# Kernel optimization log

Measured on AMD Instinct MI355X. Metric: run time of the kernel, lower is better.

Reference implementation:

```python
import jax, jax.numpy as jnp
import numpy as np

D_MODEL = 1024
N_HEADS = 16
D_K = D_MODEL // N_HEADS
THETA = 10000.0
SEQ = 2048
BATCH = 2


def setup_inputs() -> dict:
    key = jax.random.key(0)
    ks = jax.random.split(key, 5)
    std = (2.0 / (D_MODEL + D_MODEL)) ** 0.5
    return {
        "x": jax.random.normal(ks[0], (BATCH, SEQ, D_MODEL), dtype=jnp.float32),
        "token_positions": jnp.arange(SEQ, dtype=jnp.int64 if jax.config.jax_enable_x64 else jnp.int32),
        "wq": jax.random.normal(ks[1], (D_MODEL, D_MODEL), dtype=jnp.float32) * std,
        "wk": jax.random.normal(ks[2], (D_MODEL, D_MODEL), dtype=jnp.float32) * std,
        "wv": jax.random.normal(ks[3], (D_MODEL, D_MODEL), dtype=jnp.float32) * std,
        "wo": jax.random.normal(ks[4], (D_MODEL, D_MODEL), dtype=jnp.float32) * std,
    }


def _apply_rope(t, token_positions):
    # t: [b, h, s, d_k]; interleaved even/odd rotation (RoPE)
    k = jnp.arange(D_K // 2, dtype=t.dtype)
    inv_freq = THETA ** (-2.0 * k / D_K)                     # [d_k/2]
    angles = token_positions.astype(t.dtype)[:, None] * inv_freq  # [s, d_k/2]
    cos, sin = jnp.cos(angles), jnp.sin(angles)
    even, odd = t[..., 0::2], t[..., 1::2]
    re = even * cos - odd * sin
    ro = odd * cos + even * sin
    # re-interleave: stack last then reshape back to [..., d_k]
    return jnp.stack([re, ro], axis=-1).reshape(t.shape)


def reference(x, token_positions, wq, wk, wv, wo):
    b, s, _ = x.shape
    def proj(w):
        y = jnp.einsum("bsd,ed->bse", x, w)               # Linear: x @ W^T
        return y.reshape(b, s, N_HEADS, D_K).transpose(0, 2, 1, 3)  # [b,h,s,dk]
    q, k, v = proj(wq), proj(wk), proj(wv)
    q = _apply_rope(q, token_positions)
    k = _apply_rope(k, token_positions)
    scores = jnp.einsum("bhqd,bhkd->bhqk", q, k) / jnp.sqrt(jnp.asarray(D_K, x.dtype))
    attn = jax.nn.softmax(scores, axis=-1)
    out = jnp.einsum("bhqk,bhkd->bhqd", attn, v)          # [b,h,s,dk]
    out = out.transpose(0, 2, 1, 3).reshape(b, s, D_MODEL)
    return jnp.einsum("bsd,ed->bse", out, wo)
```

## Files before the change

kernel.cpp:

```cpp
#include <hip/hip_runtime.h>
#include <stdint.h>

typedef __bf16 bf16x8 __attribute__((ext_vector_type(8)));
typedef __bf16 bf16x2 __attribute__((ext_vector_type(2)));
typedef float f32x4 __attribute__((ext_vector_type(4)));
typedef float f32x16 __attribute__((ext_vector_type(16)));
typedef unsigned short ushort_t;
typedef unsigned int uint;
typedef uint uint4v __attribute__((ext_vector_type(4)));

#define SEQ    2048
#define DMODEL 1024
#define NHEAD  16
#define DKH    64
#define NBATCH 2
#define MROWS  (NBATCH*SEQ)
#define LOG2E  1.44269504088896340736f

__device__ __forceinline__ uint pk2(float a, float b) {
  bf16x2 t; t[0] = (__bf16)a; t[1] = (__bf16)b;
  return __builtin_bit_cast(uint, t);
}
__device__ __forceinline__ ushort_t b1(float a) {
  return __builtin_bit_cast(ushort_t, (__bf16)a);
}
__device__ __forceinline__ float fexp2(float x) {
#if __has_builtin(__builtin_amdgcn_exp2f)
  return __builtin_amdgcn_exp2f(x);
#else
  return exp2f(x);
#endif
}

__device__ __forceinline__ void gload16(const void* g, void* l) {
  __builtin_amdgcn_global_load_lds(
      (const __attribute__((address_space(1))) void*)g,
      (__attribute__((address_space(3))) void*)l, 16, 0, 0);
}

__device__ __forceinline__ f32x4 mfma16(bf16x8 a, bf16x8 b, f32x4 c) {
  return __builtin_amdgcn_mfma_f32_16x16x32_bf16(a, b, c, 0, 0, 0);
}
__device__ __forceinline__ f32x16 mfma32(bf16x8 a, bf16x8 b, f32x16 c) {
  return __builtin_amdgcn_mfma_f32_32x32x16_bf16(a, b, c, 0, 0, 0);
}

__global__ __launch_bounds__(256) void cvt_all(
    const float* __restrict__ x, const float* __restrict__ wq,
    const float* __restrict__ wk, const float* __restrict__ wv,
    const float* __restrict__ wo, const int* __restrict__ tokpos,
    uint2* __restrict__ out, float2* __restrict__ tab)
{
  int b = blockIdx.x;
  if (b >= 8192) {
    int t = (b - 8192) * 256 + threadIdx.x;
    int s = t >> 5, k = t & 31;
    double inv = pow(10000.0, -(double)(2 * k) / 64.0);
    double ang = (double)tokpos[s] * inv;
    tab[t] = make_float2((float)cos(ang), (float)sin(ang));
    return;
  }
  const float4* src; uint2* dst; int i;
  if (b < 4096) {
    i = b * 256 + threadIdx.x; src = (const float4*)x; dst = out;
  } else {
    int s = (b - 4096) >> 10;
    i = ((b - 4096) & 1023) * 256 + threadIdx.x;
    src = (const float4*)(s == 0 ? wq : s == 1 ? wk : s == 2 ? wv : wo);
    dst = out + (size_t)1048576 + (size_t)s * 262144;
  }
  float4 v = src[i];
  uint2 r; r.x = pk2(v.x, v.y); r.y = pk2(v.z, v.w);
  dst[i] = r;
}

__global__ __launch_bounds__(256) void gemm_nt(
    const ushort_t* __restrict__ A, const ushort_t* __restrict__ W,
    const float2* __restrict__ tab,
    ushort_t* __restrict__ Qo, ushort_t* __restrict__ Ko, ushort_t* __restrict__ Vo,
    float* __restrict__ outf, int fused, int nbx)
{
  __shared__ ushort_t lA[2][128 * 64];
  __shared__ ushort_t lB[2][128 * 64];
  const int tid = threadIdx.x;
  const int lin = blockIdx.y * nbx + blockIdx.x;
  const int nwg = nbx * gridDim.y;
  const int n = (lin & 7) * (nwg >> 3) + (lin >> 3);
  const int vbx = n % nbx, vby = n / nbx;
  const int w = tid >> 6, l = tid & 63, lo = l & 15, hi = l >> 4;
  const int wr = (w >> 1) * 64, wc = (w & 1) * 64;
  const char* Ab = (const char*)A + (size_t)vby * 128 * 2048;
  const char* Bb = (const char*)W + (size_t)vbx * 128 * 2048;
  f32x4 acc[4][4] = {};

  const int o0 = w * 1024 + l * 16;
  const int r0 = o0 >> 7;
  const int us = ((o0 >> 4) & 7) ^ (r0 & 7);
  const char* ap = Ab + (size_t)r0 * 2048 + us * 16;
  const char* bp = Bb + (size_t)r0 * 2048 + us * 16;

  auto stage = [&](char* dA, char* dB, const char* aq, const char* bq) {
    #pragma unroll
    for (int i = 0; i < 4; ++i) {
      gload16(aq + i * 65536, dA + w * 1024 + i * 4096);
      gload16(bq + i * 65536, dB + w * 1024 + i * 4096);
    }
  };
  auto comp = [&](const ushort_t* lAb, const ushort_t* lBb) {
    #pragma unroll
    for (int c = 0; c < 2; ++c) {
      bf16x8 af[4], wf[4];
      #pragma unroll
      for (int m = 0; m < 4; ++m) {
        int row = wr + m * 16 + lo;
        af[m] = *(const bf16x8*)((const char*)lAb + row * 128 + ((c * 64 + hi * 16) ^ ((row & 7) << 4)));
      }
      #pragma unroll
      for (int n2 = 0; n2 < 4; ++n2) {
        int row = wc + n2 * 16 + lo;
        wf[n2] = *(const bf16x8*)((const char*)lBb + row * 128 + ((c * 64 + hi * 16) ^ ((row & 7) << 4)));
      }
      #pragma unroll
      for (int m = 0; m < 4; ++m)
        #pragma unroll
        for (int n2 = 0; n2 < 4; ++n2)
          acc[m][n2] = mfma16(af[m], wf[n2], acc[m][n2]);
    }
  };

  stage((char*)lA[0], (char*)lB[0], ap, bp); ap += 128; bp += 128;
  #pragma unroll 1
  for (int it = 0; it < 8; ++it) {
    stage((char*)lA[1], (char*)lB[1], ap, bp); ap += 128; bp += 128;
    asm volatile("s_waitcnt vmcnt(8)" ::: "memory");
    __builtin_amdgcn_s_barrier();
    asm volatile("" ::: "memory");
    comp(lA[0], lB[0]);
    __builtin_amdgcn_s_barrier();
    asm volatile("" ::: "memory");
    if (it < 7) {
      stage((char*)lA[0], (char*)lB[0], ap, bp); ap += 128; bp += 128;
      asm volatile("s_waitcnt vmcnt(8)" ::: "memory");
    } else {
      asm volatile("s_waitcnt vmcnt(0)" ::: "memory");
    }
    __builtin_amdgcn_s_barrier();
    asm volatile("" ::: "memory");
    comp(lA[1], lB[1]);
    __builtin_amdgcn_s_barrier();
    asm volatile("" ::: "memory");
  }

  const int mode = fused ? (vbx >> 3) : 3;
  const int colblk = fused ? (vbx & 7) : vbx;
  const int rowbase = vby * 128 + wr + hi * 4;
  const int colbase = colblk * 128 + wc + lo;

  if (mode == 3) {
    #pragma unroll
    for (int m = 0; m < 4; ++m)
      #pragma unroll
      for (int n2 = 0; n2 < 4; ++n2) {
        int e = colbase + n2 * 16;
        #pragma unroll
        for (int r = 0; r < 4; ++r) {
          int row = rowbase + m * 16 + r;
          outf[(size_t)row * 1024 + e] = acc[m][n2][r];
        }
      }
    return;
  }
  if (mode == 2) {
    #pragma unroll
    for (int m = 0; m < 4; ++m) {
      int row0 = rowbase + m * 16;
      int b = row0 >> 11, s = row0 & 2047;
      int b2 = (s >> 2) & 3;
      int sp = (s & ~12) | ((b2 & 1) << 3) | ((b2 >> 1) << 2);
      #pragma unroll
      for (int n2 = 0; n2 < 4; ++n2) {
        int e = colbase + n2 * 16;
        int h = e >> 6, dk = e & 63;
        uint2 pk;
        pk.x = pk2(acc[m][n2][0], acc[m][n2][1]);
        pk.y = pk2(acc[m][n2][2], acc[m][n2][3]);
        *(uint2*)(Vo + ((size_t)((b * NHEAD + h) * DKH + dk) * SEQ + sp)) = pk;
      }
    }
    return;
  }
  ushort_t* outb = (mode == 0) ? Qo : Ko;
  const float qscale = (mode == 0) ? (0.125f * LOG2E) : 1.0f;
  #pragma unroll
  for (int m = 0; m < 4; ++m) {
    #pragma unroll
    for (int n2 = 0; n2 < 4; ++n2) {
      int e = colbase + n2 * 16;
      int h = e >> 6, dk = e & 63, kf = dk >> 1;
      float sgn = (e & 1) ? 1.0f : -1.0f;
      #pragma unroll
      for (int r = 0; r < 4; ++r) {
        int row = rowbase + m * 16 + r;
        int s = row & 2047, b = row >> 11;
        float2 cs = tab[s * 32 + kf];
        float v = acc[m][n2][r];
        float p = __shfl_xor(v, 1, 64);
        float res = (v * cs.x + sgn * p * cs.y) * qscale;
        outb[((size_t)((b * NHEAD + h) * SEQ + s)) * DKH + dk] = b1(res);
      }
    }
  }
}

__global__ __launch_bounds__(256) void attn_fwd(
    const ushort_t* __restrict__ Qg, const ushort_t* __restrict__ Kg,
    const ushort_t* __restrict__ VTg, ushort_t* __restrict__ attn)
{
  __shared__ char lds[67584];
  const int tid = threadIdx.x;
  const int w = tid >> 6, l = tid & 63;
  const int q31 = l & 31, hf = l >> 5, s7 = l & 7;
  const int lin = blockIdx.y * gridDim.x + blockIdx.x;
  const int n = (lin & 7) * 128 + (lin >> 3);
  const int bh = n >> 5;
  const int q0 = (n & 31) * 64;
  const char* Kb = (const char*)Kg + (size_t)bh * 2048 * 128;
  const char* Vb = (const char*)VTg + (size_t)bh * 64 * 4096;

  bf16x8 qreg[2][4];
  #pragma unroll
  for (int qb = 0; qb < 2; ++qb) {
    const ushort_t* qp = Qg + ((size_t)bh * 2048 + q0 + qb * 32 + q31) * 64 + hf * 8;
    #pragma unroll
    for (int c = 0; c < 4; ++c) qreg[qb][c] = *(const bf16x8*)(qp + c * 16);
  }

  f32x16 accO[2][2] = {};
  float lsum[2] = {0.f, 0.f};

  char* wlds = lds + w * 16384;
  const char* ra[4];
  #pragma unroll
  for (int c = 0; c < 4; ++c)
    ra[c] = wlds + q31 * 128 + ((c * 32 + hf * 16) ^ (s7 << 4));

  const int usw = (l & 7) ^ (l >> 3);
  const int kb0 = w * 512;
  const char* kst = Kb + (size_t)(kb0 + (l >> 3)) * 128 + usw * 16;
  const char* vst = Vb + (size_t)((l >> 3) + (usw >> 2) * 32) * 4096
                       + (size_t)kb0 * 2 + (usw & 3) * 16;

  auto stageT = [&](int slot) {
    char* sp = wlds + slot;
    #pragma unroll
    for (int i = 0; i < 4; ++i)
      gload16(kst + i * 1024, sp + i * 1024 + l * 16);
    #pragma unroll
    for (int i = 0; i < 4; ++i)
      gload16(vst + i * 32768, sp + 4096 + i * 1024 + l * 16);
    kst += 4096; vst += 64;
  };

  auto tileC = [&](int slot) {
    const int bo = slot;
    bf16x8 kf[4];
    #pragma unroll
    for (int c = 0; c < 4; ++c)
      kf[c] = *(const bf16x8*)(ra[c] + bo);
    f32x16 s0 = {}, s1 = {};
    #pragma unroll
    for (int c = 0; c < 4; ++c) {
      s0 = mfma32(kf[c], qreg[0][c], s0);
      s1 = mfma32(kf[c], qreg[1][c], s1);
    }
    float p0[16], p1[16];
    float t0 = 0.f, t1 = 0.f;
    #pragma unroll
    for (int r = 0; r < 16; ++r) { p0[r] = fexp2(s0[r]); t0 += p0[r]; }
    #pragma unroll
    for (int r = 0; r < 16; ++r) { p1[r] = fexp2(s1[r]); t1 += p1[r]; }
    lsum[0] += t0; lsum[1] += t1;
    #pragma unroll
    for (int kcl = 0; kcl < 2; ++kcl) {
      const float* a0 = p0 + kcl * 8;
      const float* a1 = p1 + kcl * 8;
      uint4v u0 = { pk2(a0[0], a0[1]), pk2(a0[2], a0[3]),
                    pk2(a0[4], a0[5]), pk2(a0[6], a0[7]) };
      uint4v u1 = { pk2(a1[0], a1[1]), pk2(a1[2], a1[3]),
                    pk2(a1[4], a1[5]), pk2(a1[6], a1[7]) };
      bf16x8 pb0 = __builtin_bit_cast(bf16x8, u0);
      bf16x8 pb1 = __builtin_bit_cast(bf16x8, u1);
      bf16x8 vf0 = *(const bf16x8*)(ra[kcl]     + bo + 4096);
      bf16x8 vf1 = *(const bf16x8*)(ra[kcl + 2] + bo + 4096);
      accO[0][0] = mfma32(vf0, pb0, accO[0][0]);
      accO[0][1] = mfma32(vf1, pb0, accO[0][1]);
      accO[1][0] = mfma32(vf0, pb1, accO[1][0]);
      accO[1][1] = mfma32(vf1, pb1, accO[1][1]);
    }
  };

  stageT(0);
  #pragma unroll 1
  for (int it = 0; it < 7; ++it) {
    asm volatile("s_waitcnt lgkmcnt(0)" ::: "memory");
    stageT(8192);
    asm volatile("s_waitcnt vmcnt(8)" ::: "memory");
    __builtin_amdgcn_sched_barrier(0);
    tileC(0);
    asm volatile("s_waitcnt lgkmcnt(0)" ::: "memory");
    stageT(0);
    asm volatile("s_waitcnt vmcnt(8)" ::: "memory");
    __builtin_amdgcn_sched_barrier(0);
    tileC(8192);
  }
  asm volatile("s_waitcnt lgkmcnt(0)" ::: "memory");
  stageT(8192);
  asm volatile("s_waitcnt vmcnt(8)" ::: "memory");
  __builtin_amdgcn_sched_barrier(0);
  tileC(0);
  asm volatile("s_waitcnt vmcnt(0)" ::: "memory");
  __builtin_amdgcn_sched_barrier(0);
  tileC(8192);

  __syncthreads();
  #pragma unroll
  for (int qb = 0; qb < 2; ++qb)
    #pragma unroll
    for (int db = 0; db < 2; ++db)
      #pragma unroll
      for (int c2 = 0; c2 < 4; ++c2) {
        int j = qb * 8 + db * 4 + c2;
        f32x4 v = { accO[qb][db][c2 * 4 + 0], accO[qb][db][c2 * 4 + 1],
                    accO[qb][db][c2 * 4 + 2], accO[qb][db][c2 * 4 + 3] };
        *(f32x4*)(lds + w * 16384 + j * 1024 + l * 16) = v;
      }
  *(float2*)(lds + 65536 + w * 512 + l * 8) = make_float2(lsum[0], lsum[1]);
  __syncthreads();

  float lt0 = 0.f, lt1 = 0.f;
  #pragma unroll
  for (int wp = 0; wp < 4; ++wp) {
    float2 lo = *(const float2*)(lds + 65536 + wp * 512 + l * 8);
    lt0 += lo.x; lt1 += lo.y;
  }
  lt0 += __shfl_xor(lt0, 32, 64);
  lt1 += __shfl_xor(lt1, 32, 64);
  float inv0 = 1.0f / lt0, inv1 = 1.0f / lt1;
  int b = bh >> 4, head = bh & 15;
  #pragma unroll
  for (int jj = 0; jj < 4; ++jj) {
    int j = w * 4 + jj;
    int qb = j >> 3, db = (j >> 2) & 1, c2 = j & 3;
    f32x4 v = {0.f, 0.f, 0.f, 0.f};
    #pragma unroll
    for (int wp = 0; wp < 4; ++wp) {
      f32x4 u = *(const f32x4*)(lds + wp * 16384 + j * 1024 + l * 16);
      v[0] += u[0]; v[1] += u[1]; v[2] += u[2]; v[3] += u[3];
    }
    float inv = qb ? inv1 : inv0;
    int d0 = db * 32 + c2 * 8 + hf * 4;
    ushort_t* op = attn + (size_t)(b * 2048 + q0 + qb * 32 + q31) * 1024 + head * 64;
    uint2 pk;
    pk.x = pk2(v[0] * inv, v[1] * inv);
    pk.y = pk2(v[2] * inv, v[3] * inv);
    *(uint2*)(op + d0) = pk;
  }
}

extern "C" void kernel_launch(void* const* d_in, const int* in_sizes, int n_in,
                              void* d_out, int out_size, void* d_ws, size_t ws_size,
                              hipStream_t stream) {
  const float* x  = (const float*)d_in[0];
  const int* tok  = (const int*)d_in[1];
  const float* wq = (const float*)d_in[2];
  const float* wk = (const float*)d_in[3];
  const float* wv = (const float*)d_in[4];
  const float* wo = (const float*)d_in[5];
  float* out = (float*)d_out;
  char* ws = (char*)d_ws;

  size_t off = 0;
  float2* tab = (float2*)(ws + off); off += (size_t)SEQ * 32 * sizeof(float2);
  ushort_t* xb  = (ushort_t*)(ws + off); off += (size_t)MROWS * DMODEL * 2;
  ushort_t* wqkv = (ushort_t*)(ws + off); off += (size_t)3 * DMODEL * DMODEL * 2;
  ushort_t* wob = (ushort_t*)(ws + off); off += (size_t)DMODEL * DMODEL * 2;
  ushort_t* Qg  = (ushort_t*)(ws + off); off += (size_t)MROWS * DMODEL * 2;
  ushort_t* Kg  = (ushort_t*)(ws + off); off += (size_t)MROWS * DMODEL * 2;
  ushort_t* VTg = (ushort_t*)(ws + off); off += (size_t)MROWS * DMODEL * 2;
  ushort_t* attnb = xb;
  if (ws_size < off) return;

  cvt_all<<<8448, 256, 0, stream>>>(x, wq, wk, wv, wo, tok, (uint2*)xb, tab);

  gemm_nt<<<dim3(24, 32), 256, 0, stream>>>(xb, wqkv, tab, Qg, Kg, VTg, nullptr, 1, 24);

  attn_fwd<<<dim3(SEQ / 64, NBATCH * NHEAD), 256, 0, stream>>>(Qg, Kg, VTg, attnb);

  gemm_nt<<<dim3(8, 32), 256, 0, stream>>>(attnb, wob, nullptr, nullptr, nullptr, nullptr, out, 0, 8);
}
```

Before: 119.0 us.

## Software-pipeline attention inner loop, overlapping next QK with current PV

Splits the per-tile attention body into QK^T MFMA, exp/pack and PV MFMA stages, then reorders the loop so the QK scores for the next K/V tile are computed alongside the PV accumulation for the current one. Both LDS slots are staged up front, and the vmcnt waits are relaxed so each wait covers only the K half of the newest stage. The sched_barriers that serialized each tile are removed. The aim is to hide the exp/softmax latency and the memory waits behind MFMA work, at the cost of more live registers for the carried scores and packed probabilities.

```diff
diff --git a/kernel.cpp b/kernel.cpp
--- a/kernel.cpp
+++ b/kernel.cpp
@@ -261,18 +261,22 @@
     kst += 4096; vst += 64;
   };
 
-  auto tileC = [&](int slot) {
-    const int bo = slot;
+  f32x16 s0, s1;
+  bf16x8 pb[2][2];
+
+  auto tileQK = [&](int slot) {
     bf16x8 kf[4];
     #pragma unroll
     for (int c = 0; c < 4; ++c)
-      kf[c] = *(const bf16x8*)(ra[c] + bo);
-    f32x16 s0 = {}, s1 = {};
+      kf[c] = *(const bf16x8*)(ra[c] + slot);
+    s0 = (f32x16){}; s1 = (f32x16){};
     #pragma unroll
     for (int c = 0; c < 4; ++c) {
       s0 = mfma32(kf[c], qreg[0][c], s0);
       s1 = mfma32(kf[c], qreg[1][c], s1);
     }
+  };
+  auto packP = [&]() {
     float p0[16], p1[16];
     float t0 = 0.f, t1 = 0.f;
     #pragma unroll
@@ -288,39 +292,48 @@
                     pk2(a0[4], a0[5]), pk2(a0[6], a0[7]) };
       uint4v u1 = { pk2(a1[0], a1[1]), pk2(a1[2], a1[3]),
                     pk2(a1[4], a1[5]), pk2(a1[6], a1[7]) };
-      bf16x8 pb0 = __builtin_bit_cast(bf16x8, u0);
-      bf16x8 pb1 = __builtin_bit_cast(bf16x8, u1);
-      bf16x8 vf0 = *(const bf16x8*)(ra[kcl]     + bo + 4096);
-      bf16x8 vf1 = *(const bf16x8*)(ra[kcl + 2] + bo + 4096);
-      accO[0][0] = mfma32(vf0, pb0, accO[0][0]);
-      accO[0][1] = mfma32(vf1, pb0, accO[0][1]);
-      accO[1][0] = mfma32(vf0, pb1, accO[1][0]);
-      accO[1][1] = mfma32(vf1, pb1, accO[1][1]);
+      pb[0][kcl] = __builtin_bit_cast(bf16x8, u0);
+      pb[1][kcl] = __builtin_bit_cast(bf16x8, u1);
+    }
+  };
+  auto tilePV = [&](int slot) {
+    #pragma unroll
+    for (int kcl = 0; kcl < 2; ++kcl) {
+      bf16x8 vf0 = *(const bf16x8*)(ra[kcl]     + slot + 4096);
+      bf16x8 vf1 = *(const bf16x8*)(ra[kcl + 2] + slot + 4096);
+      accO[0][0] = mfma32(vf0, pb[0][kcl], accO[0][0]);
+      accO[0][1] = mfma32(vf1, pb[0][kcl], accO[0][1]);
+      accO[1][0] = mfma32(vf0, pb[1][kcl], accO[1][0]);
+      accO[1][1] = mfma32(vf1, pb[1][kcl], accO[1][1]);
     }
   };
 
   stageT(0);
+  stageT(8192);
+  asm volatile("s_waitcnt vmcnt(8)" ::: "memory");
+  tileQK(0);
+  packP();
   #pragma unroll 1
   for (int it = 0; it < 7; ++it) {
+    asm volatile("s_waitcnt vmcnt(4)" ::: "memory");
+    tileQK(8192);
+    tilePV(0);
+    packP();
+    asm volatile("s_waitcnt lgkmcnt(0)" ::: "memory");
+    stageT(0);
+    asm volatile("s_waitcnt vmcnt(4)" ::: "memory");
+    tileQK(0);
+    tilePV(8192);
+    packP();
     asm volatile("s_waitcnt lgkmcnt(0)" ::: "memory");
     stageT(8192);
-    asm volatile("s_waitcnt vmcnt(8)" ::: "memory");
-    __builtin_amdgcn_sched_barrier(0);
-    tileC(0);
-    asm volatile("s_waitcnt lgkmcnt(0)" ::: "memory");
-    stageT(0);
-    asm volatile("s_waitcnt vmcnt(8)" ::: "memory");
-    __builtin_amdgcn_sched_barrier(0);
-    tileC(8192);
-  }
-  asm volatile("s_waitcnt lgkmcnt(0)" ::: "memory");
-  stageT(8192);
-  asm volatile("s_waitcnt vmcnt(8)" ::: "memory");
-  __builtin_amdgcn_sched_barrier(0);
-  tileC(0);
+  }
+  asm volatile("s_waitcnt vmcnt(4)" ::: "memory");
+  tileQK(8192);
+  tilePV(0);
+  packP();
   asm volatile("s_waitcnt vmcnt(0)" ::: "memory");
-  __builtin_amdgcn_sched_barrier(0);
-  tileC(8192);
+  tilePV(8192);
 
   __syncthreads();
   #pragma unroll
```

Measured after the change: 127.0 us. +6.7%, slower.

## Load K/V fragments directly from global memory and shrink LDS for occupancy

Applied to the files above, without the earlier changes.

The attention kernel drops the double-buffered, async LDS staging of K and V tiles. Each wave now reads its K and V MFMA fragments straight from global memory (through L2/L1) in a plainly unrolled loop. The cross-wave reduction becomes a two-level tree, which halves shared memory, and launch bounds now request 3 blocks per CU to raise occupancy. The trade is uncoalesced, cache-dependent global loads with no explicit prefetch overlap, in exchange for less LDS traffic and more resident waves.

```diff
diff --git a/kernel.cpp b/kernel.cpp
--- a/kernel.cpp
+++ b/kernel.cpp
@@ -212,14 +212,14 @@
   }
 }
 
-__global__ __launch_bounds__(256) void attn_fwd(
+__global__ __launch_bounds__(256, 3) void attn_fwd(
     const ushort_t* __restrict__ Qg, const ushort_t* __restrict__ Kg,
     const ushort_t* __restrict__ VTg, ushort_t* __restrict__ attn)
 {
-  __shared__ char lds[67584];
+  __shared__ char lds[33792];
   const int tid = threadIdx.x;
   const int w = tid >> 6, l = tid & 63;
-  const int q31 = l & 31, hf = l >> 5, s7 = l & 7;
+  const int q31 = l & 31, hf = l >> 5;
   const int lin = blockIdx.y * gridDim.x + blockIdx.x;
   const int n = (lin & 7) * 128 + (lin >> 3);
   const int bh = n >> 5;
@@ -238,35 +238,17 @@
   f32x16 accO[2][2] = {};
   float lsum[2] = {0.f, 0.f};
 
-  char* wlds = lds + w * 16384;
-  const char* ra[4];
-  #pragma unroll
-  for (int c = 0; c < 4; ++c)
-    ra[c] = wlds + q31 * 128 + ((c * 32 + hf * 16) ^ (s7 << 4));
-
-  const int usw = (l & 7) ^ (l >> 3);
   const int kb0 = w * 512;
-  const char* kst = Kb + (size_t)(kb0 + (l >> 3)) * 128 + usw * 16;
-  const char* vst = Vb + (size_t)((l >> 3) + (usw >> 2) * 32) * 4096
-                       + (size_t)kb0 * 2 + (usw & 3) * 16;
-
-  auto stageT = [&](int slot) {
-    char* sp = wlds + slot;
-    #pragma unroll
-    for (int i = 0; i < 4; ++i)
-      gload16(kst + i * 1024, sp + i * 1024 + l * 16);
-    #pragma unroll
-    for (int i = 0; i < 4; ++i)
-      gload16(vst + i * 32768, sp + 4096 + i * 1024 + l * 16);
-    kst += 4096; vst += 64;
-  };
-
-  auto tileC = [&](int slot) {
-    const int bo = slot;
+  const char* kbase = Kb + (size_t)(kb0 + q31) * 128 + hf * 16;
+  const char* vbase = Vb + (size_t)q31 * 4096 + (size_t)kb0 * 2 + hf * 16;
+
+  #pragma unroll 2
+  for (int step = 0; step < 16; ++step) {
+    const char* kp = kbase + step * 4096;
     bf16x8 kf[4];
     #pragma unroll
     for (int c = 0; c < 4; ++c)
-      kf[c] = *(const bf16x8*)(ra[c] + bo);
+      kf[c] = *(const bf16x8*)(kp + c * 32);
     f32x16 s0 = {}, s1 = {};
     #pragma unroll
     for (int c = 0; c < 4; ++c) {
@@ -280,6 +262,7 @@
     #pragma unroll
     for (int r = 0; r < 16; ++r) { p1[r] = fexp2(s1[r]); t1 += p1[r]; }
     lsum[0] += t0; lsum[1] += t1;
+    const char* vp = vbase + step * 64;
     #pragma unroll
     for (int kcl = 0; kcl < 2; ++kcl) {
       const float* a0 = p0 + kcl * 8;
@@ -290,80 +273,127 @@
                     pk2(a1[4], a1[5]), pk2(a1[6], a1[7]) };
       bf16x8 pb0 = __builtin_bit_cast(bf16x8, u0);
       bf16x8 pb1 = __builtin_bit_cast(bf16x8, u1);
-      bf16x8 vf0 = *(const bf16x8*)(ra[kcl]     + bo + 4096);
-      bf16x8 vf1 = *(const bf16x8*)(ra[kcl + 2] + bo + 4096);
+      bf16x8 vf0 = *(const bf16x8*)(vp + kcl * 32);
+      bf16x8 vf1 = *(const bf16x8*)(vp + 131072 + kcl * 32);
       accO[0][0] = mfma32(vf0, pb0, accO[0][0]);
       accO[0][1] = mfma32(vf1, pb0, accO[0][1]);
       accO[1][0] = mfma32(vf0, pb1, accO[1][0]);
       accO[1][1] = mfma32(vf1, pb1, accO[1][1]);
     }
-  };
-
-  stageT(0);
-  #pragma unroll 1
-  for (int it = 0; it < 7; ++it) {
-    asm volatile("s_waitcnt lgkmcnt(0)" ::: "memory");
-    stageT(8192);
-    asm volatile("s_waitcnt vmcnt(8)" ::: "memory");
-    __builtin_amdgcn_sched_barrier(0);
-    tileC(0);
-    asm volatile("s_waitcnt lgkmcnt(0)" ::: "memory");
-    stageT(0);
-    asm volatile("s_waitcnt vmcnt(8)" ::: "memory");
-    __builtin_amdgcn_sched_barrier(0);
-    tileC(8192);
-  }
-  asm volatile("s_waitcnt lgkmcnt(0)" ::: "memory");
-  stageT(8192);
-  asm volatile("s_waitcnt vmcnt(8)" ::: "memory");
-  __builtin_amdgcn_sched_barrier(0);
-  tileC(0);
-  asm volatile("s_waitcnt vmcnt(0)" ::: "memory");
-  __builtin_amdgcn_sched_barrier(0);
-  tileC(8192);
-
+  }
+
+  if (w >= 2) {
+    char* dst = lds + (w - 2) * 16384;
+    #pragma unroll
+    for (int qb = 0; qb < 2; ++qb)
+      #pragma unroll
+      for (int db = 0; db < 2; ++db)
+        #pragma unroll
+        for (int c2 = 0; c2 < 4; ++c2) {
+          int j = qb * 8 + db * 4 + c2;
+          f32x4 v = { accO[qb][db][c2 * 4 + 0], accO[qb][db][c2 * 4 + 1],
+                      accO[qb][db][c2 * 4 + 2], accO[qb][db][c2 * 4 + 3] };
+          *(f32x4*)(dst + j * 1024 + l * 16) = v;
+        }
+    *(float2*)(lds + 32768 + (w - 2) * 512 + l * 8) = make_float2(lsum[0], lsum[1]);
+  }
   __syncthreads();
-  #pragma unroll
-  for (int qb = 0; qb < 2; ++qb)
+  if (w < 2) {
+    const char* srcp = lds + w * 16384;
+    #pragma unroll
+    for (int qb = 0; qb < 2; ++qb)
+      #pragma unroll
+      for (int db = 0; db < 2; ++db)
+        #pragma unroll
+        for (int c2 = 0; c2 < 4; ++c2) {
+          int j = qb * 8 + db * 4 + c2;
+          f32x4 v = *(const f32x4*)(srcp + j * 1024 + l * 16);
+          accO[qb][db][c2 * 4 + 0] += v[0];
+          accO[qb][db][c2 * 4 + 1] += v[1];
+          accO[qb][db][c2 * 4 + 2] += v[2];
+          accO[qb][db][c2 * 4 + 3] += v[3];
+        }
+    float2 lo = *(const float2*)(lds + 32768 + w * 512 + l * 8);
+    lsum[0] += lo.x; lsum[1] += lo.y;
+  }
+  __syncthreads();
+  if (w == 0) {
     #pragma unroll
     for (int db = 0; db < 2; ++db)
       #pragma unroll
       for (int c2 = 0; c2 < 4; ++c2) {
-        int j = qb * 8 + db * 4 + c2;
-        f32x4 v = { accO[qb][db][c2 * 4 + 0], accO[qb][db][c2 * 4 + 1],
-                    accO[qb][db][c2 * 4 + 2], accO[qb][db][c2 * 4 + 3] };
-        *(f32x4*)(lds + w * 16384 + j * 1024 + l * 16) = v;
-      }
-  *(float2*)(lds + 65536 + w * 512 + l * 8) = make_float2(lsum[0], lsum[1]);
+        int j = db * 4 + c2;
+        f32x4 v = { accO[1][db][c2 * 4 + 0], accO[1][db][c2 * 4 + 1],
+                    accO[1][db][c2 * 4 + 2], accO[1][db][c2 * 4 + 3] };
+        *(f32x4*)(lds + j * 1024 + l * 16) = v;
+      }
+    *(float*)(lds + 32768 + l * 4) = lsum[1];
+  } else if (w == 1) {
+    #pragma unroll
+    for (int db = 0; db < 2; ++db)
+      #pragma unroll
+      for (int c2 = 0; c2 < 4; ++c2) {
+        int j = db * 4 + c2;
+        f32x4 v = { accO[0][db][c2 * 4 + 0], accO[0][db][c2 * 4 + 1],
+                    accO[0][db][c2 * 4 + 2], accO[0][db][c2 * 4 + 3] };
+        *(f32x4*)(lds + 8192 + j * 1024 + l * 16) = v;
+      }
+    *(float*)(lds + 32768 + 512 + l * 4) = lsum[0];
+  }
   __syncthreads();
-
-  float lt0 = 0.f, lt1 = 0.f;
-  #pragma unroll
-  for (int wp = 0; wp < 4; ++wp) {
-    float2 lo = *(const float2*)(lds + 65536 + wp * 512 + l * 8);
-    lt0 += lo.x; lt1 += lo.y;
-  }
-  lt0 += __shfl_xor(lt0, 32, 64);
-  lt1 += __shfl_xor(lt1, 32, 64);
-  float inv0 = 1.0f / lt0, inv1 = 1.0f / lt1;
   int b = bh >> 4, head = bh & 15;
-  #pragma unroll
-  for (int jj = 0; jj < 4; ++jj) {
-    int j = w * 4 + jj;
-    int qb = j >> 3, db = (j >> 2) & 1, c2 = j & 3;
-    f32x4 v = {0.f, 0.f, 0.f, 0.f};
-    #pragma unroll
-    for (int wp = 0; wp < 4; ++wp) {
-      f32x4 u = *(const f32x4*)(lds + wp * 16384 + j * 1024 + l * 16);
-      v[0] += u[0]; v[1] += u[1]; v[2] += u[2]; v[3] += u[3];
-    }
-    float inv = qb ? inv1 : inv0;
-    int d0 = db * 32 + c2 * 8 + hf * 4;
-    ushort_t* op = attn + (size_t)(b * 2048 + q0 + qb * 32 + q31) * 1024 + head * 64;
-    uint2 pk;
-    pk.x = pk2(v[0] * inv, v[1] * inv);
-    pk.y = pk2(v[2] * inv, v[3] * inv);
-    *(uint2*)(op + d0) = pk;
+  if (w == 0) {
+    #pragma unroll
+    for (int db = 0; db < 2; ++db)
+      #pragma unroll
+      for (int c2 = 0; c2 < 4; ++c2) {
+        int j = db * 4 + c2;
+        f32x4 v = *(const f32x4*)(lds + 8192 + j * 1024 + l * 16);
+        accO[0][db][c2 * 4 + 0] += v[0];
+        accO[0][db][c2 * 4 + 1] += v[1];
+        accO[0][db][c2 * 4 + 2] += v[2];
+        accO[0][db][c2 * 4 + 3] += v[3];
+      }
+    lsum[0] += *(const float*)(lds + 32768 + 512 + l * 4);
+    float lt = lsum[0] + __shfl_xor(lsum[0], 32, 64);
+    float inv = 1.0f / lt;
+    ushort_t* op = attn + (size_t)(b * 2048 + q0 + q31) * 1024 + head * 64;
+    #pragma unroll
+    for (int db = 0; db < 2; ++db)
+      #pragma unroll
+      for (int m = 0; m < 4; ++m) {
+        int d0 = db * 32 + m * 8 + hf * 4;
+        uint2 pk;
+        pk.x = pk2(accO[0][db][m * 4 + 0] * inv, accO[0][db][m * 4 + 1] * inv);
+        pk.y = pk2(accO[0][db][m * 4 + 2] * inv, accO[0][db][m * 4 + 3] * inv);
+        *(uint2*)(op + d0) = pk;
+      }
+  } else if (w == 1) {
+    #pragma unroll
+    for (int db = 0; db < 2; ++db)
+      #pragma unroll
+      for (int c2 = 0; c2 < 4; ++c2) {
+        int j = db * 4 + c2;
+        f32x4 v = *(const f32x4*)(lds + j * 1024 + l * 16);
+        accO[1][db][c2 * 4 + 0] += v[0];
+        accO[1][db][c2 * 4 + 1] += v[1];
+        accO[1][db][c2 * 4 + 2] += v[2];
+        accO[1][db][c2 * 4 + 3] += v[3];
+      }
+    lsum[1] += *(const float*)(lds + 32768 + l * 4);
+    float lt = lsum[1] + __shfl_xor(lsum[1], 32, 64);
+    float inv = 1.0f / lt;
+    ushort_t* op = attn + (size_t)(b * 2048 + q0 + 32 + q31) * 1024 + head * 64;
+    #pragma unroll
+    for (int db = 0; db < 2; ++db)
+      #pragma unroll
+      for (int m = 0; m < 4; ++m) {
+        int d0 = db * 32 + m * 8 + hf * 4;
+        uint2 pk;
+        pk.x = pk2(accO[1][db][m * 4 + 0] * inv, accO[1][db][m * 4 + 1] * inv);
+        pk.y = pk2(accO[1][db][m * 4 + 2] * inv, accO[1][db][m * 4 + 3] * inv);
+        *(uint2*)(op + d0) = pk;
+      }
   }
 }
 
```

New measurement: 163.1 us. 37.0% more time.
